# Optimization experiments

Hardware: AMD Instinct MI355X
Metric: run time of the kernel (lower is better)

## Reference

```python
import jax, jax.numpy as jnp
import numpy as np

TOPK, NPRO, NALP, NADS = 13, 31, 24, 37
ALPHA, BETA, EPS = 1.0, 6.0, 1e-9
BS, NA, NM = 32, 8400, 64
IMG = 640.0


def _make_boxes(key, shape, img=IMG):
    k1, k2 = jax.random.split(key)
    cxy = jax.random.uniform(k1, shape[:-1] + (2,), minval=0.0, maxval=img)
    wh = jax.random.uniform(k2, shape[:-1] + (2,), minval=10.0, maxval=120.0)
    return jnp.concatenate([cxy - wh / 2, cxy + wh / 2], axis=-1)


def setup_inputs() -> dict:
    key = jax.random.key(0)
    ks = jax.random.split(key, 12)
    pd_pro_scores = jax.random.uniform(ks[0], (BS, NA, NPRO))
    pd_alp_scores = jax.random.uniform(ks[1], (BS, NA, NALP))
    pd_ads_scores = jax.random.uniform(ks[2], (5, BS, NA, NADS))
    pd_bboxes = _make_boxes(ks[3], (BS, NA, 4))
    pd_corners = jax.random.uniform(ks[4], (BS, NA, 8), maxval=IMG)
    anc_points = jax.random.uniform(ks[5], (NA, 2), maxval=IMG)
    gt_pro = jax.random.randint(ks[6], (BS, NM, 1), 0, NPRO, dtype=jnp.int32)
    gt_alp = jax.random.randint(ks[7], (BS, NM, 1), 0, NALP, dtype=jnp.int32)
    gt_ads = jax.random.randint(ks[8], (BS, NM, 5), 0, NADS, dtype=jnp.int32)
    gt_bboxes = _make_boxes(ks[9], (BS, NM, 4))
    gt_corners = jax.random.uniform(ks[10], (BS, NM, 8), maxval=IMG)
    nvalid = jax.random.randint(ks[11], (BS,), NM // 2, NM + 1)
    mask_gt = (jnp.arange(NM)[None, :] < nvalid[:, None]).astype(jnp.float32)[..., None]
    return {"pd_pro_scores": pd_pro_scores, "pd_alp_scores": pd_alp_scores,
            "pd_ads_scores": pd_ads_scores, "pd_bboxes": pd_bboxes,
            "pd_corners": pd_corners, "anc_points": anc_points,
            "gt_pro": gt_pro, "gt_alp": gt_alp, "gt_ads": gt_ads,
            "gt_bboxes": gt_bboxes, "gt_corners": gt_corners, "mask_gt": mask_gt}


def _iou(gt, pd):
    # gt: (bs, nm, 4) xyxy; pd: (bs, na, 4) xyxy -> (bs, nm, na)
    g, p = gt[:, :, None, :], pd[:, None, :, :]
    lt = jnp.maximum(g[..., :2], p[..., :2])
    rb = jnp.minimum(g[..., 2:], p[..., 2:])
    inter = jnp.clip(rb - lt, 0).prod(-1)
    a1 = jnp.clip(g[..., 2:] - g[..., :2], 0).prod(-1)
    a2 = jnp.clip(p[..., 2:] - p[..., :2], 0).prod(-1)
    return inter / (a1 + a2 - inter + EPS)


def reference(pd_pro_scores, pd_alp_scores, pd_ads_scores, pd_bboxes, pd_corners,
              anc_points, gt_pro, gt_alp, gt_ads, gt_bboxes, gt_corners, mask_gt):
    bs, na = pd_pro_scores.shape[:2]
    nm = gt_bboxes.shape[1]
    b = jnp.arange(bs)[:, None]

    # --- get_box_metrics ---
    labels = gt_pro[..., 0].astype(jnp.int32)                       # (bs, nm)
    bbox_scores = pd_pro_scores.transpose(0, 2, 1)[b, labels]       # (bs, nm, na)
    overlaps = _iou(gt_bboxes, pd_bboxes)                           # (bs, nm, na)
    align = (bbox_scores ** ALPHA) * (overlaps ** BETA)

    # --- select_candidates_in_gts ---
    xy = anc_points[None, None]                                     # (1,1,na,2)
    d_lt = xy - gt_bboxes[:, :, None, :2]
    d_rb = gt_bboxes[:, :, None, 2:] - xy
    mask_in = (jnp.minimum(d_lt, d_rb).min(-1) > EPS).astype(align.dtype)

    # --- select_topk_candidates ---
    metrics = align * mask_in
    _, tidx = jax.lax.top_k(metrics, TOPK)                          # (bs, nm, topk)
    valid = mask_gt[..., 0] > 0                                     # (bs, nm)
    tidx = jnp.where(valid[..., None], tidx, 0)
    rows = jnp.arange(bs * nm)[:, None]
    counts = jnp.zeros((bs * nm, na), jnp.int32).at[rows, tidx.reshape(bs * nm, TOPK)].add(1)
    counts = counts.reshape(bs, nm, na)
    is_in_topk = jnp.where(counts > 1, 0, counts).astype(metrics.dtype)
    mask_pos = is_in_topk * mask_in * mask_gt                       # (bs, nm, na)

    # --- select_highest_overlaps ---
    fg_mask = mask_pos.sum(-2)                                      # (bs, na)
    multi = fg_mask > 1
    max_idx = overlaps.argmax(1)                                    # (bs, na)
    is_max = (jnp.arange(nm)[None, :, None] == max_idx[:, None, :]).astype(mask_pos.dtype)
    mask_pos = jnp.where(multi[:, None, :], is_max, mask_pos)
    fg_mask = mask_pos.sum(-2)
    target_gt_idx = mask_pos.argmax(-2)                             # (bs, na)

    # --- get_targets ---
    target_pro = jnp.maximum(gt_pro[..., 0].astype(jnp.int32)[b, target_gt_idx], 0)
    target_alp = jnp.maximum(gt_alp[..., 0].astype(jnp.int32)[b, target_gt_idx], 0)
    target_ads = jnp.maximum(gt_ads.astype(jnp.int32)[b, target_gt_idx], 0)   # (bs, na, 5)
    target_ad0_4 = jnp.moveaxis(target_ads, -1, 0)                  # (5, bs, na)
    target_bboxes = gt_bboxes[b, target_gt_idx]                     # (bs, na, 4)
    target_corners = gt_corners[b, target_gt_idx]                   # (bs, na, 8)

    fg = (fg_mask > 0).astype(jnp.float32)                          # (bs, na)
    pro_scores = jax.nn.one_hot(target_pro, NPRO, dtype=jnp.float32) * fg[..., None]
    alp_scores = jax.nn.one_hot(target_alp, NALP, dtype=jnp.float32) * fg[..., None]
    ads_scores = jax.nn.one_hot(target_ad0_4, NADS, dtype=jnp.float32) * fg[None, :, :, None]

    # --- normalization of pro scores ---
    align = align * mask_pos
    pos_align = align.max(-1, keepdims=True)                        # (bs, nm, 1)
    pos_ov = (overlaps * mask_pos).max(-1, keepdims=True)           # (bs, nm, 1)
    norm = (align * pos_ov / (pos_align + EPS)).max(-2)[..., None]  # (bs, na, 1)
    pro_scores = pro_scores * norm

    return (target_pro, target_alp, target_ad0_4, target_bboxes, target_corners,
            pro_scores, alp_scores, ads_scores, fg_mask > 0)
```

## Files before the change

### kernel.cpp

```cpp
#include <hip/hip_runtime.h>
#include <cstdint>
#include <cstddef>

#define BS 32
#define NA 8400
#define NM 64
#define NPRO 31
#define NALP 24
#define NADS 37
#define TOPK 13
#define FEPS 1e-9f
#define WORDS 264
#define CAP 1024
#define TL 16

#define OFF0 0L
#define OFF1 268800L
#define OFF2 537600L
#define OFF3 1881600L
#define OFF4 2956800L
#define OFF5 5107200L
#define OFF6 13440000L
#define OFF7 19891200L
#define OFF8 69619200L

typedef float f4_t __attribute__((ext_vector_type(4)));

__device__ __forceinline__ void nt4(float* p, float a, float b, float c, float d) {
  f4_t v = {a, b, c, d};
  __builtin_nontemporal_store(v, (f4_t*)p);
}
__device__ __forceinline__ void nt1(float* p, float v) {
  __builtin_nontemporal_store(v, p);
}

__device__ __forceinline__ float iou1(float4 g, float ga, float4 p, float pa) {
  float iw = fmaxf(fminf(g.z, p.z) - fmaxf(g.x, p.x), 0.f);
  float ih = fmaxf(fminf(g.w, p.w) - fmaxf(g.y, p.y), 0.f);
  float inter = iw * ih;
  return inter / (ga + pa - inter + FEPS);
}

__global__ __launch_bounds__(256) void kA(
    const float* __restrict__ pro, const float* __restrict__ pd_bb,
    const float* __restrict__ anc, const int* __restrict__ gt_pro,
    const float* __restrict__ gt_bb, const float* __restrict__ mask_gt,
    short* __restrict__ tlist, unsigned* __restrict__ posA,
    unsigned* __restrict__ posO)
{
  __shared__ unsigned s_in[WORDS];
  __shared__ unsigned s_pos[WORDS];
  __shared__ float s_cv[CAP];
  __shared__ int   s_ci[CAP];
  __shared__ int   s_cnt;

  const int bm = blockIdx.x;
  const int b = bm >> 6;
  const int tid = threadIdx.x;

  if (tid == 0) { posA[bm] = 0u; posO[bm] = 0u; }

  short* tl = tlist + bm * TL;
  if (!(mask_gt[bm] > 0.f)) {
    if (tid == 0) tl[0] = 0;
    return;
  }

  for (int w = tid; w < WORDS; w += 256) { s_in[w] = 0u; s_pos[w] = 0u; }
  if (tid == 0) s_cnt = 0;
  __syncthreads();

  const float4 g = *(const float4*)(gt_bb + (size_t)bm * 4);
  const int label = gt_pro[bm];
  const float ga = fmaxf(g.z - g.x, 0.f) * fmaxf(g.w - g.y, 0.f);
  const float* pb = pd_bb + (size_t)b * NA * 4;
  const float* ps = pro + (size_t)b * NA * NPRO + label;

  for (int a = tid; a < NA; a += 256) {
    float2 ap = *(const float2*)(anc + 2 * a);
    float din = fminf(fminf(ap.x - g.x, ap.y - g.y), fminf(g.z - ap.x, g.w - ap.y));
    if (din > FEPS) {
      atomicOr(&s_in[a >> 5], 1u << (a & 31));
      float4 p = *(const float4*)(pb + (size_t)a * 4);
      float pa = fmaxf(p.z - p.x, 0.f) * fmaxf(p.w - p.y, 0.f);
      float iou = iou1(g, ga, p, pa);
      float i2 = iou * iou;
      float met = ps[(size_t)a * NPRO] * (i2 * i2 * i2);
      if (met > 0.f) {
        atomicOr(&s_pos[a >> 5], 1u << (a & 31));
        int pidx = atomicAdd(&s_cnt, 1);
        if (pidx < CAP) { s_cv[pidx] = met; s_ci[pidx] = a; }
      }
    }
  }
  __syncthreads();

  const int P = min(s_cnt, CAP);
  if (tid < 64) {
    float lv[16]; int li[16];
#pragma unroll
    for (int e = 0; e < 16; e++) {
      int p = tid + e * 64;
      bool ok = p < P;
      lv[e] = ok ? s_cv[p] : -1.f;
      li[e] = ok ? s_ci[p] : NA;
    }
    const int nsel = min(P, TOPK);
    for (int k = 0; k < nsel; k++) {
      float bv = -1.f; int bi = NA;
#pragma unroll
      for (int e = 0; e < 16; e++)
        if (lv[e] > bv || (lv[e] == bv && li[e] < bi)) { bv = lv[e]; bi = li[e]; }
      for (int s = 1; s < 64; s <<= 1) {
        float ov = __shfl_xor(bv, s);
        int   oi = __shfl_xor(bi, s);
        if (ov > bv || (ov == bv && oi < bi)) { bv = ov; bi = oi; }
      }
#pragma unroll
      for (int e = 0; e < 16; e++) if (li[e] == bi) lv[e] = -1.f;
      if (tid == 0) tl[1 + k] = (short)bi;
    }
    if (tid == 0) {
      int cnt = nsel;
      if (P < TOPK) {
        int need = TOPK - P;
        for (int a = 0; a < NA && need > 0; a++) {
          if (!((s_pos[a >> 5] >> (a & 31)) & 1u)) {
            need--;
            if ((s_in[a >> 5] >> (a & 31)) & 1u) tl[1 + cnt++] = (short)a;
          }
        }
      }
      tl[0] = (short)cnt;
    }
  }
}

__global__ __launch_bounds__(256) void kB(
    const float* __restrict__ pro, const float* __restrict__ pd_bb,
    const int* __restrict__ gt_pro, const float* __restrict__ gt_bb,
    const short* __restrict__ tlist,
    unsigned* __restrict__ posA, unsigned* __restrict__ posO,
    int* __restrict__ tgi, float* __restrict__ fgo, float* __restrict__ avo)
{
  __shared__ float4 s_g[NM];
  __shared__ float s_ga[NM];
  __shared__ int s_lab[NM];
  __shared__ unsigned long long s_m[256];
  __shared__ short s_tl[NM * TL];

  const int b = blockIdx.y;
  const int a0 = blockIdx.x << 8;
  const int tid = threadIdx.x;

  s_m[tid] = 0ull;
  if (tid < NM) {
    float4 gg = *(const float4*)(gt_bb + (size_t)(b * NM + tid) * 4);
    s_g[tid] = gg;
    s_ga[tid] = fmaxf(gg.z - gg.x, 0.f) * fmaxf(gg.w - gg.y, 0.f);
    s_lab[tid] = gt_pro[b * NM + tid];
  }
  for (int i = tid; i < NM * TL / 2; i += 256)
    ((int*)s_tl)[i] = ((const int*)(tlist + (size_t)b * NM * TL))[i];
  __syncthreads();

  for (int i = tid; i < NM * TL; i += 256) {
    int m = i >> 4, sl = i & 15;
    if (sl >= 1 && sl <= (int)s_tl[m * TL]) {
      int ai = s_tl[i];
      unsigned d = (unsigned)(ai - a0);
      if (d < 256u) atomicOr(&s_m[d], 1ull << m);
    }
  }
  __syncthreads();

  const int a = a0 + tid;
  if (a >= NA) return;

  const int ia = b * NA + a;
  unsigned long long msk = s_m[tid];
  int cnt = __popcll(msk);
  int chosen = 0; float ovv = 0.f, av = 0.f, fg = 0.f;

  if (cnt > 0) {
    fg = 1.f;
    float4 p = *(const float4*)(pd_bb + (size_t)ia * 4);
    float pa = fmaxf(p.z - p.x, 0.f) * fmaxf(p.w - p.y, 0.f);
    if (cnt == 1) {
      chosen = __ffsll(msk) - 1;
      ovv = iou1(s_g[chosen], s_ga[chosen], p, pa);
    } else {
      float best = -1.f; int bmx = 0;
      for (int m = 0; m < NM; m++) {
        float v = iou1(s_g[m], s_ga[m], p, pa);
        if (v > best) { best = v; bmx = m; }
      }
      chosen = bmx; ovv = best;
    }
    float sc = pro[(size_t)ia * NPRO + s_lab[chosen]];
    float o2 = ovv * ovv;
    av = sc * (o2 * o2 * o2);
    atomicMax(&posA[b * NM + chosen], __float_as_uint(av));
    atomicMax(&posO[b * NM + chosen], __float_as_uint(ovv));
  }
  tgi[ia] = chosen; fgo[ia] = fg; avo[ia] = av;
}

__global__ __launch_bounds__(256) void kC(
    const int* __restrict__ gt_pro, const int* __restrict__ gt_alp,
    const int* __restrict__ gt_ads, const float* __restrict__ gt_bb,
    const float* __restrict__ gt_cor,
    const unsigned* __restrict__ posA, const unsigned* __restrict__ posO,
    const int* __restrict__ tgi, const float* __restrict__ fgi,
    const float* __restrict__ avi, float* __restrict__ out)
{
  __shared__ int s_tp[256], s_ta[256];
  __shared__ int s_td[5][256];
  __shared__ float s_pv[256], s_fg[256];

  const int b = blockIdx.y;
  const int a0 = blockIdx.x * 256;
  const int tid = threadIdx.x;
  const int na = min(256, NA - a0);
  const int a = a0 + tid;

  if (a < NA) {
    const int ia = b * NA + a;
    const int g = tgi[ia];
    const float fg = fgi[ia];
    float no = 0.f;
    if (fg > 0.f) {
      no = avi[ia] * __uint_as_float(posO[b * NM + g]) /
           (__uint_as_float(posA[b * NM + g]) + FEPS);
    }
    const int gi = b * NM + g;
    const int tp = gt_pro[gi], ta = gt_alp[gi];
    s_tp[tid] = tp; s_ta[tid] = ta; s_pv[tid] = no; s_fg[tid] = fg;
    nt1(out + OFF0 + ia, (float)tp);
    nt1(out + OFF1 + ia, (float)ta);
#pragma unroll
    for (int k = 0; k < 5; k++) {
      int td = gt_ads[(size_t)gi * 5 + k];
      s_td[k][tid] = td;
      nt1(out + OFF2 + (size_t)k * (BS * NA) + ia, (float)td);
    }
    float4 bb = *(const float4*)(gt_bb + (size_t)gi * 4);
    nt4(out + OFF3 + (size_t)ia * 4, bb.x, bb.y, bb.z, bb.w);
    float4 c0 = *(const float4*)(gt_cor + (size_t)gi * 8);
    float4 c1 = *(const float4*)(gt_cor + (size_t)gi * 8 + 4);
    nt4(out + OFF4 + (size_t)ia * 8, c0.x, c0.y, c0.z, c0.w);
    nt4(out + OFF4 + (size_t)ia * 8 + 4, c1.x, c1.y, c1.z, c1.w);
    nt1(out + OFF8 + ia, fg);
  }
  __syncthreads();

  {
    float* dst = out + OFF5 + ((size_t)b * NA + a0) * NPRO;
    const int n = na * NPRO;
    for (int e4 = tid * 4; e4 < n; e4 += 1024) {
      float vv[4];
#pragma unroll
      for (int j = 0; j < 4; j++) {
        int e = e4 + j; int al = e / NPRO; int c = e - al * NPRO;
        vv[j] = (c == s_tp[al]) ? s_pv[al] : 0.f;
      }
      nt4(dst + e4, vv[0], vv[1], vv[2], vv[3]);
    }
  }
  {
    float* dst = out + OFF6 + ((size_t)b * NA + a0) * NALP;
    const int n = na * NALP;
    for (int e4 = tid * 4; e4 < n; e4 += 1024) {
      float vv[4];
#pragma unroll
      for (int j = 0; j < 4; j++) {
        int e = e4 + j; int al = e / NALP; int c = e - al * NALP;
        vv[j] = (c == s_ta[al]) ? s_fg[al] : 0.f;
      }
      nt4(dst + e4, vv[0], vv[1], vv[2], vv[3]);
    }
  }
#pragma unroll
  for (int k = 0; k < 5; k++) {
    float* dst = out + OFF7 + (size_t)k * ((size_t)BS * NA * NADS) +
                 ((size_t)b * NA + a0) * NADS;
    const int n = na * NADS;
    for (int e4 = tid * 4; e4 < n; e4 += 1024) {
      float vv[4];
#pragma unroll
      for (int j = 0; j < 4; j++) {
        int e = e4 + j; int al = e / NADS; int c = e - al * NADS;
        vv[j] = (c == s_td[k][al]) ? s_fg[al] : 0.f;
      }
      nt4(dst + e4, vv[0], vv[1], vv[2], vv[3]);
    }
  }
}

extern "C" void kernel_launch(void* const* d_in, const int* in_sizes, int n_in,
                              void* d_out, int out_size, void* d_ws, size_t ws_size,
                              hipStream_t stream) {
  const float* pd_pro  = (const float*)d_in[0];
  const float* pd_bb   = (const float*)d_in[3];
  const float* anc     = (const float*)d_in[5];
  const int*   gt_pro  = (const int*)d_in[6];
  const int*   gt_alp  = (const int*)d_in[7];
  const int*   gt_ads  = (const int*)d_in[8];
  const float* gt_bb   = (const float*)d_in[9];
  const float* gt_cor  = (const float*)d_in[10];
  const float* mask_gt = (const float*)d_in[11];
  float* out = (float*)d_out;

  char* ws = (char*)d_ws;
  short*    tlist = (short*)(ws);
  unsigned* posA  = (unsigned*)(ws + 65536);
  unsigned* posO  = (unsigned*)(ws + 73728);
  int*      tgi   = (int*)     (ws + 81920);
  float*    fgo   = (float*)   (ws + 1157120);
  float*    avo   = (float*)   (ws + 2232320);

  kA<<<BS * NM, 256, 0, stream>>>(pd_pro, pd_bb, anc, gt_pro, gt_bb, mask_gt,
                                  tlist, posA, posO);
  dim3 gridBC((NA + 255) / 256, BS);
  kB<<<gridBC, 256, 0, stream>>>(pd_pro, pd_bb, gt_pro, gt_bb, tlist,
                                 posA, posO, tgi, fgo, avo);
  kC<<<gridBC, 256, 0, stream>>>(gt_pro, gt_alp, gt_ads, gt_bb, gt_cor,
                                 posA, posO, tgi, fgo, avo, out);
}
```

Baseline: 135.5 us.

## Use wave ballots for candidate compaction, shrink kC blocks, drop nontemporal stores

In kA, per-anchor shared atomics for the inside and positive bitmaps and the candidate counter are replaced by wave-level ballots. Each wave writes its bitmap words directly and reserves candidate slots with a single atomicAdd. The candidate cap and per-lane top-k arrays are halved. kC now runs 64-thread blocks over 64 anchors, and its output writes switch from nontemporal stores to plain stores. Halving the cap risks dropping candidates if more than 512 anchors are positive for one GT, and plain stores may pollute cache on the large one-hot output.

Measured after the change: 121.1 us, median of 2. 10.6% less time.

```diff
diff --git a/kernel.cpp b/kernel.cpp
--- a/kernel.cpp
+++ b/kernel.cpp
@@ -11,7 +11,7 @@
 #define TOPK 13
 #define FEPS 1e-9f
 #define WORDS 264
-#define CAP 1024
+#define CAP 512
 #define TL 16
 
 #define OFF0 0L
@@ -23,16 +23,6 @@
 #define OFF6 13440000L
 #define OFF7 19891200L
 #define OFF8 69619200L
-
-typedef float f4_t __attribute__((ext_vector_type(4)));
-
-__device__ __forceinline__ void nt4(float* p, float a, float b, float c, float d) {
-  f4_t v = {a, b, c, d};
-  __builtin_nontemporal_store(v, (f4_t*)p);
-}
-__device__ __forceinline__ void nt1(float* p, float v) {
-  __builtin_nontemporal_store(v, p);
-}
 
 __device__ __forceinline__ float iou1(float4 g, float ga, float4 p, float pa) {
   float iw = fmaxf(fminf(g.z, p.z) - fmaxf(g.x, p.x), 0.f);
@@ -57,17 +47,15 @@
   const int bm = blockIdx.x;
   const int b = bm >> 6;
   const int tid = threadIdx.x;
-
-  if (tid == 0) { posA[bm] = 0u; posO[bm] = 0u; }
+  const int lane = tid & 63;
+
+  if (tid == 0) { posA[bm] = 0u; posO[bm] = 0u; s_cnt = 0; }
 
   short* tl = tlist + bm * TL;
   if (!(mask_gt[bm] > 0.f)) {
     if (tid == 0) tl[0] = 0;
     return;
   }
-
-  for (int w = tid; w < WORDS; w += 256) { s_in[w] = 0u; s_pos[w] = 0u; }
-  if (tid == 0) s_cnt = 0;
   __syncthreads();
 
   const float4 g = *(const float4*)(gt_bb + (size_t)bm * 4);
@@ -76,20 +64,38 @@
   const float* pb = pd_bb + (size_t)b * NA * 4;
   const float* ps = pro + (size_t)b * NA * NPRO + label;
 
-  for (int a = tid; a < NA; a += 256) {
-    float2 ap = *(const float2*)(anc + 2 * a);
-    float din = fminf(fminf(ap.x - g.x, ap.y - g.y), fminf(g.z - ap.x, g.w - ap.y));
-    if (din > FEPS) {
-      atomicOr(&s_in[a >> 5], 1u << (a & 31));
-      float4 p = *(const float4*)(pb + (size_t)a * 4);
-      float pa = fmaxf(p.z - p.x, 0.f) * fmaxf(p.w - p.y, 0.f);
-      float iou = iou1(g, ga, p, pa);
-      float i2 = iou * iou;
-      float met = ps[(size_t)a * NPRO] * (i2 * i2 * i2);
-      if (met > 0.f) {
-        atomicOr(&s_pos[a >> 5], 1u << (a & 31));
-        int pidx = atomicAdd(&s_cnt, 1);
-        if (pidx < CAP) { s_cv[pidx] = met; s_ci[pidx] = a; }
+  for (int j = 0; j < (NA + 255) / 256; j++) {
+    const int a = j * 256 + tid;
+    bool inb = false, posb = false; float met = 0.f;
+    if (a < NA) {
+      float2 ap = *(const float2*)(anc + 2 * a);
+      float din = fminf(fminf(ap.x - g.x, ap.y - g.y), fminf(g.z - ap.x, g.w - ap.y));
+      if (din > FEPS) {
+        inb = true;
+        float4 p = *(const float4*)(pb + (size_t)a * 4);
+        float pa = fmaxf(p.z - p.x, 0.f) * fmaxf(p.w - p.y, 0.f);
+        float iou = iou1(g, ga, p, pa);
+        float i2 = iou * iou;
+        met = ps[(size_t)a * NPRO] * (i2 * i2 * i2);
+        posb = met > 0.f;
+      }
+    }
+    unsigned long long bin  = __ballot(inb);
+    unsigned long long bpos = __ballot(posb);
+    if (lane == 0) {
+      int w0 = (j << 3) + ((tid >> 6) << 1);
+      s_in[w0]      = (unsigned)bin;
+      s_in[w0 + 1]  = (unsigned)(bin >> 32);
+      s_pos[w0]     = (unsigned)bpos;
+      s_pos[w0 + 1] = (unsigned)(bpos >> 32);
+    }
+    if (bpos) {
+      int base = 0;
+      if (lane == 0) base = atomicAdd(&s_cnt, __popcll(bpos));
+      base = __shfl(base, 0);
+      if (posb) {
+        int idx = base + __popcll(bpos & ((1ull << lane) - 1ull));
+        if (idx < CAP) { s_cv[idx] = met; s_ci[idx] = a; }
       }
     }
   }
@@ -97,9 +103,9 @@
 
   const int P = min(s_cnt, CAP);
   if (tid < 64) {
-    float lv[16]; int li[16];
-#pragma unroll
-    for (int e = 0; e < 16; e++) {
+    float lv[8]; int li[8];
+#pragma unroll
+    for (int e = 0; e < 8; e++) {
       int p = tid + e * 64;
       bool ok = p < P;
       lv[e] = ok ? s_cv[p] : -1.f;
@@ -109,7 +115,7 @@
     for (int k = 0; k < nsel; k++) {
       float bv = -1.f; int bi = NA;
 #pragma unroll
-      for (int e = 0; e < 16; e++)
+      for (int e = 0; e < 8; e++)
         if (lv[e] > bv || (lv[e] == bv && li[e] < bi)) { bv = lv[e]; bi = li[e]; }
       for (int s = 1; s < 64; s <<= 1) {
         float ov = __shfl_xor(bv, s);
@@ -117,7 +123,7 @@
         if (ov > bv || (ov == bv && oi < bi)) { bv = ov; bi = oi; }
       }
 #pragma unroll
-      for (int e = 0; e < 16; e++) if (li[e] == bi) lv[e] = -1.f;
+      for (int e = 0; e < 8; e++) if (li[e] == bi) lv[e] = -1.f;
       if (tid == 0) tl[1 + k] = (short)bi;
     }
     if (tid == 0) {
@@ -206,7 +212,7 @@
   tgi[ia] = chosen; fgo[ia] = fg; avo[ia] = av;
 }
 
-__global__ __launch_bounds__(256) void kC(
+__global__ __launch_bounds__(64) void kC(
     const int* __restrict__ gt_pro, const int* __restrict__ gt_alp,
     const int* __restrict__ gt_ads, const float* __restrict__ gt_bb,
     const float* __restrict__ gt_cor,
@@ -214,17 +220,17 @@
     const int* __restrict__ tgi, const float* __restrict__ fgi,
     const float* __restrict__ avi, float* __restrict__ out)
 {
-  __shared__ int s_tp[256], s_ta[256];
-  __shared__ int s_td[5][256];
-  __shared__ float s_pv[256], s_fg[256];
+  __shared__ int s_tp[64], s_ta[64];
+  __shared__ int s_td[5][64];
+  __shared__ float s_pv[64], s_fg[64];
 
   const int b = blockIdx.y;
-  const int a0 = blockIdx.x * 256;
+  const int a0 = blockIdx.x * 64;
   const int tid = threadIdx.x;
-  const int na = min(256, NA - a0);
+  const int na = min(64, NA - a0);
   const int a = a0 + tid;
 
-  if (a < NA) {
+  if (tid < na) {
     const int ia = b * NA + a;
     const int g = tgi[ia];
     const float fg = fgi[ia];
@@ -236,48 +242,48 @@
     const int gi = b * NM + g;
     const int tp = gt_pro[gi], ta = gt_alp[gi];
     s_tp[tid] = tp; s_ta[tid] = ta; s_pv[tid] = no; s_fg[tid] = fg;
-    nt1(out + OFF0 + ia, (float)tp);
-    nt1(out + OFF1 + ia, (float)ta);
+    out[OFF0 + ia] = (float)tp;
+    out[OFF1 + ia] = (float)ta;
 #pragma unroll
     for (int k = 0; k < 5; k++) {
       int td = gt_ads[(size_t)gi * 5 + k];
       s_td[k][tid] = td;
-      nt1(out + OFF2 + (size_t)k * (BS * NA) + ia, (float)td);
+      out[OFF2 + (size_t)k * (BS * NA) + ia] = (float)td;
     }
     float4 bb = *(const float4*)(gt_bb + (size_t)gi * 4);
-    nt4(out + OFF3 + (size_t)ia * 4, bb.x, bb.y, bb.z, bb.w);
+    *(float4*)(out + OFF3 + (size_t)ia * 4) = bb;
     float4 c0 = *(const float4*)(gt_cor + (size_t)gi * 8);
     float4 c1 = *(const float4*)(gt_cor + (size_t)gi * 8 + 4);
-    nt4(out + OFF4 + (size_t)ia * 8, c0.x, c0.y, c0.z, c0.w);
-    nt4(out + OFF4 + (size_t)ia * 8 + 4, c1.x, c1.y, c1.z, c1.w);
-    nt1(out + OFF8 + ia, fg);
+    *(float4*)(out + OFF4 + (size_t)ia * 8) = c0;
+    *(float4*)(out + OFF4 + (size_t)ia * 8 + 4) = c1;
+    out[OFF8 + ia] = fg;
   }
   __syncthreads();
 
   {
     float* dst = out + OFF5 + ((size_t)b * NA + a0) * NPRO;
     const int n = na * NPRO;
-    for (int e4 = tid * 4; e4 < n; e4 += 1024) {
+    for (int e4 = tid * 4; e4 < n; e4 += 256) {
       float vv[4];
 #pragma unroll
       for (int j = 0; j < 4; j++) {
         int e = e4 + j; int al = e / NPRO; int c = e - al * NPRO;
         vv[j] = (c == s_tp[al]) ? s_pv[al] : 0.f;
       }
-      nt4(dst + e4, vv[0], vv[1], vv[2], vv[3]);
+      *(float4*)(dst + e4) = make_float4(vv[0], vv[1], vv[2], vv[3]);
     }
   }
   {
     float* dst = out + OFF6 + ((size_t)b * NA + a0) * NALP;
     const int n = na * NALP;
-    for (int e4 = tid * 4; e4 < n; e4 += 1024) {
+    for (int e4 = tid * 4; e4 < n; e4 += 256) {
       float vv[4];
 #pragma unroll
       for (int j = 0; j < 4; j++) {
         int e = e4 + j; int al = e / NALP; int c = e - al * NALP;
         vv[j] = (c == s_ta[al]) ? s_fg[al] : 0.f;
       }
-      nt4(dst + e4, vv[0], vv[1], vv[2], vv[3]);
+      *(float4*)(dst + e4) = make_float4(vv[0], vv[1], vv[2], vv[3]);
     }
   }
 #pragma unroll
@@ -285,14 +291,14 @@
     float* dst = out + OFF7 + (size_t)k * ((size_t)BS * NA * NADS) +
                  ((size_t)b * NA + a0) * NADS;
     const int n = na * NADS;
-    for (int e4 = tid * 4; e4 < n; e4 += 1024) {
+    for (int e4 = tid * 4; e4 < n; e4 += 256) {
       float vv[4];
 #pragma unroll
       for (int j = 0; j < 4; j++) {
         int e = e4 + j; int al = e / NADS; int c = e - al * NADS;
         vv[j] = (c == s_td[k][al]) ? s_fg[al] : 0.f;
       }
-      nt4(dst + e4, vv[0], vv[1], vv[2], vv[3]);
+      *(float4*)(dst + e4) = make_float4(vv[0], vv[1], vv[2], vv[3]);
     }
   }
 }
@@ -321,9 +327,10 @@
 
   kA<<<BS * NM, 256, 0, stream>>>(pd_pro, pd_bb, anc, gt_pro, gt_bb, mask_gt,
                                   tlist, posA, posO);
-  dim3 gridBC((NA + 255) / 256, BS);
-  kB<<<gridBC, 256, 0, stream>>>(pd_pro, pd_bb, gt_pro, gt_bb, tlist,
-                                 posA, posO, tgi, fgo, avo);
-  kC<<<gridBC, 256, 0, stream>>>(gt_pro, gt_alp, gt_ads, gt_bb, gt_cor,
-                                 posA, posO, tgi, fgo, avo, out);
-}
+  dim3 gridB((NA + 255) / 256, BS);
+  kB<<<gridB, 256, 0, stream>>>(pd_pro, pd_bb, gt_pro, gt_bb, tlist,
+                                posA, posO, tgi, fgo, avo);
+  dim3 gridC((NA + 63) / 64, BS);
+  kC<<<gridC, 64, 0, stream>>>(gt_pro, gt_alp, gt_ads, gt_bb, gt_cor,
+                               posA, posO, tgi, fgo, avo, out);
+}
```
